# Performance work log

Hardware: AMD Instinct MI355X
Metric: run time of the kernel (lower is better)

## Reference

```python
import jax, jax.numpy as jnp
import numpy as np

C_NUM, D_NUM = 64, 128
N_NODES = C_NUM * D_NUM + C_NUM + D_NUM  # 8384
HEADS, OUT = 4, 256


def gat_conv(h, src, dst, W, al, ar, b):
    """DGL-style GATConv (eval mode, attn_drop off). h:[N,F], W:[F,H*O], al/ar:[H,O], b:[H*O]."""
    N = h.shape[0]
    H, O = al.shape
    feat = (h @ W).reshape(N, H, O)
    el = jnp.sum(feat * al, axis=-1)                      # [N,H]
    er = jnp.sum(feat * ar, axis=-1)
    e = jax.nn.leaky_relu(el[src] + er[dst], 0.2)         # [E,H]
    m = jax.ops.segment_max(e, dst, num_segments=N)
    m = jnp.where(jnp.isfinite(m), m, 0.0)
    p = jnp.exp(e - m[dst])
    s = jax.ops.segment_sum(p, dst, num_segments=N)
    a = p / jnp.maximum(s[dst], 1e-9)                     # edge softmax per dst, per head
    out = jax.ops.segment_sum(a[:, :, None] * feat[src], dst, num_segments=N)  # [N,H,O]
    return out + b.reshape(1, H, O)


def cagat_layer(edges, dfeat, cvec, gw, al, ar, gb,
                wq_w, wq_b, wk_w, wk_b, wv_w, wv_b, ip_w, ip_b, op_w, op_b):
    ch = cvec.shape[1]
    pad = jnp.repeat(cvec, D_NUM, axis=0)                       # [c*d, ch]
    pad3 = jnp.broadcast_to(cvec.mean(axis=0), (D_NUM, ch))      # [d, ch]
    cfin = jnp.concatenate([pad, cvec, pad3], axis=0)            # [N, ch]
    inf = jnp.concatenate([dfeat, cfin], axis=1)                 # [N, F+ch]
    # 4 relation-specific GATConvs, stacked (HeteroGraphConv aggregate='stack')
    rst = jnp.stack([gat_conv(inf, edges[t, 0], edges[t, 1], gw[t], al[t], ar[t], gb[t])
                     for t in range(4)], axis=1)                 # [N,4,H,O]
    N = inf.shape[0]
    rst = rst.reshape(N, 4 * HEADS, OUT)
    E = OUT
    Q = (cfin @ wq_w + wq_b)[:, None, :]                         # [N,1,E]
    K = rst @ wk_w + wk_b                                        # [N,16,E]
    V = rst @ wv_w + wv_b
    # nn.MultiheadAttention(E, 1): in-proj then single-head SDPA then out-proj
    q = Q @ ip_w[:E].T + ip_b[:E]
    k = K @ ip_w[E:2 * E].T + ip_b[E:2 * E]
    v = V @ ip_w[2 * E:].T + ip_b[2 * E:]
    att = jax.nn.softmax(jnp.einsum('nqe,nke->nqk', q, k) / jnp.sqrt(jnp.float32(E)), axis=-1)
    o = jnp.einsum('nqk,nke->nqe', att, v) @ op_w.T + op_b
    return o.reshape(N, E)


def setup_inputs() -> dict:
    key = jax.random.key(0)
    ks = iter(jax.random.split(key, 64))
    rn = lambda shape: jax.random.normal(next(ks), shape, jnp.float32) * 0.05
    inp = {}
    inp['x'] = rn((D_NUM, 256))
    inp['cf'] = rn((C_NUM, 512))
    inp['cf_net_w'] = rn((512, 128)); inp['cf_net_b'] = rn((128,))
    inp['ht_w'] = rn((512, 256)); inp['ht_b'] = rn((256,))
    for l in ('1', '2'):
        inp['gw' + l] = rn((4, 384, HEADS * OUT))
        inp['al' + l] = rn((4, HEADS, OUT))
        inp['ar' + l] = rn((4, HEADS, OUT))
        inp['gb' + l] = rn((4, HEADS * OUT))
        inp['wq' + l + '_w'] = rn((128, 256)); inp['wq' + l + '_b'] = rn((256,))
        inp['wk' + l + '_w'] = rn((256, 256)); inp['wk' + l + '_b'] = rn((256,))
        inp['wv' + l + '_w'] = rn((256, 256)); inp['wv' + l + '_b'] = rn((256,))
        inp['ip' + l + '_w'] = rn((768, 256)); inp['ip' + l + '_b'] = rn((768,))
        inp['op' + l + '_w'] = rn((256, 256)); inp['op' + l + '_b'] = rn((256,))
    inp['edges'] = jax.random.randint(next(ks), (4, 2, 50000), 0, N_NODES, dtype=jnp.int32)
    return inp


def reference(x, cf, cf_net_w, cf_net_b, ht_w, ht_b,
              gw1, al1, ar1, gb1, wq1_w, wq1_b, wk1_w, wk1_b, wv1_w, wv1_b, ip1_w, ip1_b, op1_w, op1_b,
              gw2, al2, ar2, gb2, wq2_w, wq2_b, wk2_w, wk2_b, wv2_w, wv2_b, ip2_w, ip2_b, op2_w, op2_b,
              edges):
    cf_vec = cf @ cf_net_w + cf_net_b                           # [c, cell_hidden]
    d_pad = jnp.tile(x, (C_NUM, 1))                             # [c*d, in]
    d_uc = cf @ ht_w + ht_b                                     # [c, in]
    d_feat = jnp.concatenate([d_pad, d_uc, x], axis=0)          # [N, in]
    h = cagat_layer(edges, d_feat, cf_vec, gw1, al1, ar1, gb1,
                    wq1_w, wq1_b, wk1_w, wk1_b, wv1_w, wv1_b, ip1_w, ip1_b, op1_w, op1_b)
    h = cagat_layer(edges, h, cf_vec, gw2, al2, ar2, gb2,
                    wq2_w, wq2_b, wk2_w, wk2_b, wv2_w, wv2_b, ip2_w, ip2_b, op2_w, op2_b)
    return h
```

## Files before the change

kernel.cpp:

```cpp
#include <hip/hip_runtime.h>
#include <hip/hip_bf16.h>

typedef __hip_bfloat16 bf16;
typedef __attribute__((ext_vector_type(8))) short short8;
typedef __attribute__((ext_vector_type(4))) short short4v;
typedef __attribute__((ext_vector_type(4))) float f32x4;

#define KN 8384
#define KNPAD 8448
#define KE 50000
#define NBIG 4480

__device__ __forceinline__ float toF(float v){ return v; }
__device__ __forceinline__ float toF(bf16 v){ return __bfloat162float(v); }
__device__ __forceinline__ float b2f(short u){ return __uint_as_float(((unsigned int)(unsigned short)u) << 16); }
__device__ __forceinline__ void stor(float* p, float v){ *p = v; }
__device__ __forceinline__ void stor(bf16* p, float v){ *p = __float2bfloat16(v); }

__device__ __forceinline__ void glds16(const bf16* g, bf16* l){
  __builtin_amdgcn_global_load_lds(
      (const __attribute__((address_space(1))) unsigned int*)(g),
      (__attribute__((address_space(3))) unsigned int*)(l), 16, 0, 0);
}

template<typename TC>
__global__ __launch_bounds__(256)
void gemm_mfma_bt(const bf16* __restrict__ A, const bf16* __restrict__ BT,
                  const float* __restrict__ bias, TC* __restrict__ C,
                  int M, int N, int K, int ldc)
{
  __shared__ bf16 As[128 * 32];
  __shared__ bf16 Bs[128 * 32];
  const int bm = blockIdx.y * 128, bn = blockIdx.x * 128;
  const int tid = threadIdx.x;
  const int w = tid >> 6, l = tid & 63;
  const int wr = (w >> 1) * 64, wc = (w & 1) * 64;
  const int lr = l & 15;
  int rS[2], lqS[2];
  #pragma unroll
  for (int i = 0; i < 2; i++){
    rS[i] = w * 32 + i * 16 + (l >> 2);
    lqS[i] = (l & 3) ^ ((rS[i] >> 1) & 3);
  }
  const bf16* gA0 = A  + (size_t)(bm + rS[0]) * K + lqS[0] * 8;
  const bf16* gA1 = A  + (size_t)(bm + rS[1]) * K + lqS[1] * 8;
  const bf16* gB0 = BT + (size_t)(bn + rS[0]) * K + lqS[0] * 8;
  const bf16* gB1 = BT + (size_t)(bn + rS[1]) * K + lqS[1] * 8;
  bf16* lA0 = &As[w * 1024];
  bf16* lA1 = &As[w * 1024 + 512];
  bf16* lB0 = &Bs[w * 1024];
  bf16* lB1 = &Bs[w * 1024 + 512];
  f32x4 acc[4][4] = {};
  for (int k0 = 0; k0 < K; k0 += 32) {
    glds16(gA0 + k0, lA0);
    glds16(gA1 + k0, lA1);
    glds16(gB0 + k0, lB0);
    glds16(gB1 + k0, lB1);
    __syncthreads();
    short8 a[4], b[4];
    #pragma unroll
    for (int i = 0; i < 4; i++){
      int R = wr + i * 16 + lr;
      int pq = (l >> 4) ^ ((R >> 1) & 3);
      a[i] = *(short8*)&As[R * 32 + pq * 8];
    }
    #pragma unroll
    for (int j = 0; j < 4; j++){
      int R = wc + j * 16 + lr;
      int pq = (l >> 4) ^ ((R >> 1) & 3);
      b[j] = *(short8*)&Bs[R * 32 + pq * 8];
    }
    #pragma unroll
    for (int i = 0; i < 4; i++)
      #pragma unroll
      for (int j = 0; j < 4; j++)
        acc[i][j] = __builtin_amdgcn_mfma_f32_16x16x32_bf16(a[i], b[j], acc[i][j], 0, 0, 0);
    __syncthreads();
  }
  const int orow = (l >> 4) * 4, ocol = l & 15;
  #pragma unroll
  for (int i = 0; i < 4; i++){
    #pragma unroll
    for (int j = 0; j < 4; j++){
      int gcol = bn + wc + j * 16 + ocol;
      float bv = bias ? bias[gcol] : 0.f;
      #pragma unroll
      for (int rg = 0; rg < 4; rg++){
        int grow = bm + wr + i * 16 + orow + rg;
        if (grow < M) stor(&C[(size_t)grow * ldc + gcol], acc[i][j][rg] + bv);
      }
    }
  }
}

__global__ void k_transGW(const float* __restrict__ gw, bf16* __restrict__ bigBT){
  __shared__ float t[32][33];
  int rel = blockIdx.z;
  const float* B = gw + (size_t)rel * 384 * 1024;
  bf16* BT = bigBT + (size_t)rel * 1024 * 384;
  int n0 = blockIdx.x * 32, k0 = blockIdx.y * 32;
  int tx = threadIdx.x, ty = threadIdx.y;
  for (int i = ty; i < 32; i += 8)
    t[i][tx] = B[(size_t)(k0 + i) * 1024 + n0 + tx];
  __syncthreads();
  for (int i = ty; i < 32; i += 8)
    BT[(size_t)(n0 + i) * 384 + k0 + tx] = __float2bfloat16(t[tx][i]);
}

__global__ __launch_bounds__(256)
void k_galr(const float* __restrict__ gw, const float* __restrict__ al,
            const float* __restrict__ ar, bf16* __restrict__ bigBT){
  int r = blockIdx.y;
  int k = blockIdx.x * 4 + (threadIdx.x >> 6);
  int lane = threadIdx.x & 63;
  int rr = r & 15, t = rr >> 2, h = rr & 3;
  const float* wsrc = ((r < 16) ? al : ar) + t * 1024 + h * 256;
  const float* gp = gw + (size_t)t * 384 * 1024 + (size_t)k * 1024 + h * 256;
  float v = 0.f;
  #pragma unroll
  for (int i = 0; i < 4; i++){
    int o = lane + i * 64;
    v += gp[o] * wsrc[o];
  }
  #pragma unroll
  for (int off = 32; off; off >>= 1) v += __shfl_down(v, off);
  if (lane == 0) bigBT[(size_t)(4352 + r) * 384 + k] = __float2bfloat16(v);
}

__global__ void k_zpad(bf16* bigBT){
  int i = blockIdx.x * blockDim.x + threadIdx.x;
  if (i < 96 * 384) bigBT[(size_t)4384 * 384 + i] = __float2bfloat16(0.f);
}

__global__ void k_wprep(const float* __restrict__ ipw, const float* __restrict__ wkw,
                        const float* __restrict__ opw, const float* __restrict__ wvw,
                        float* __restrict__ ipwQT, float* __restrict__ wkwT,
                        float* __restrict__ opwT, float* __restrict__ wvwT){
  __shared__ float t[32][33];
  const float* S; float* D;
  switch (blockIdx.z){
    case 0: S = ipw; D = ipwQT; break;
    case 1: S = wkw; D = wkwT; break;
    case 2: S = opw; D = opwT; break;
    default: S = wvw; D = wvwT; break;
  }
  int c0 = blockIdx.x * 32, r0 = blockIdx.y * 32;
  int tx = threadIdx.x, ty = threadIdx.y;
  for (int i = ty; i < 32; i += 8)
    t[i][tx] = S[(size_t)(r0 + i) * 256 + c0 + tx];
  __syncthreads();
  for (int i = ty; i < 32; i += 8)
    D[(size_t)(c0 + i) * 256 + r0 + tx] = t[tx][i];
}

__global__ __launch_bounds__(256)
void k_fold1(const float* __restrict__ wqw, const float* __restrict__ wqb,
             const float* __restrict__ ipw, const float* __restrict__ ipb,
             const float* __restrict__ ipwQT, const float* __restrict__ wkwT,
             const float* __restrict__ opwT,
             float* __restrict__ Wq, float* __restrict__ B2,
             float* __restrict__ M1, float* __restrict__ bq){
  int b = blockIdx.x, tid = threadIdx.x;
  if (b < 128){
    int c = b; float s = 0.f;
    for (int e = 0; e < 256; e++) s += wqw[c * 256 + e] * ipwQT[e * 256 + tid];
    Wq[c * 256 + tid] = s;
  } else if (b < 384){
    int j = b - 128; float s = 0.f;
    for (int e = 0; e < 256; e++) s += wkwT[e * 256 + tid] * ipw[(256 + j) * 256 + e];
    B2[j * 256 + tid] = s;
  } else if (b < 640){
    int e = b - 384; float s = 0.f;
    for (int f = 0; f < 256; f++) s += ipw[(512 + f) * 256 + e] * opwT[f * 256 + tid];
    M1[e * 256 + tid] = s;
  } else {
    float s = 0.f;
    for (int e = 0; e < 256; e++) s += wqb[e] * ipwQT[e * 256 + tid];
    bq[tid] = s + ipb[tid];
  }
}

__global__ __launch_bounds__(256)
void k_fold2(const float* __restrict__ Wq, const float* __restrict__ B2,
             const float* __restrict__ M1, const float* __restrict__ bq,
             const float* __restrict__ wvb, const float* __restrict__ ipb,
             const float* __restrict__ opb,
             const float* __restrict__ wvwT, const float* __restrict__ opwT,
             bf16* __restrict__ bigBT, bf16* __restrict__ WvT,
             float* __restrict__ bv, float* __restrict__ biasc){
  int b = blockIdx.x, tid = threadIdx.x;
  if (b < 256){
    int d = b; float s = 0.f;
    for (int j = 0; j < 256; j++) s += Wq[d * 256 + j] * B2[j * 256 + tid];
    bigBT[(size_t)(4096 + tid) * 384 + 256 + d] = __float2bfloat16(s);
  } else if (b < 512){
    int j = b - 256; float s = 0.f;
    for (int e = 0; e < 256; e++) s += wvwT[e * 256 + tid] * M1[e * 256 + j];
    WvT[j * 256 + tid] = __float2bfloat16(s);
  } else {
    float b2 = 0.f;
    for (int j = 0; j < 256; j++) b2 += bq[j] * B2[j * 256 + tid];
    float s = 0.f;
    for (int e = 0; e < 256; e++) s += wvb[e] * M1[e * 256 + tid];
    for (int f = 0; f < 256; f++) s += ipb[512 + f] * opwT[f * 256 + tid];
    bv[tid] = s + opb[tid];
    for (int i = tid; i < NBIG; i += 256)
      biasc[i] = (i - 4096 == tid) ? b2 : 0.f;
    for (int k = 0; k < 256; k++)
      bigBT[(size_t)(4096 + tid) * 384 + k] = __float2bfloat16(0.f);
  }
}

__global__ __launch_bounds__(384)
void k_pre(const float* __restrict__ cf, const float* __restrict__ cfw, const float* __restrict__ cfb,
           const float* __restrict__ htw, const float* __restrict__ htb,
           float* __restrict__ cfvec, float* __restrict__ duc)
{
  int c = blockIdx.x;
  int col = threadIdx.x;
  __shared__ float row[512];
  for (int i = col; i < 512; i += 384) row[i] = cf[c * 512 + i];
  __syncthreads();
  if (col < 128){
    float acc = cfb[col];
    for (int k = 0; k < 512; k++) acc += row[k] * cfw[k * 128 + col];
    cfvec[c * 128 + col] = acc;
  } else {
    int j = col - 128;
    float acc = htb[j];
    for (int k = 0; k < 512; k++) acc += row[k] * htw[k * 256 + j];
    duc[c * 256 + j] = acc;
  }
}
__global__ void k_mean(const float* cv, float* m){
  int o = threadIdx.x;
  float s = 0.f;
  for (int c = 0; c < 64; c++) s += cv[c * 128 + o];
  m[o] = s * (1.f / 64.f);
}
__global__ __launch_bounds__(384)
void k_infasm(const float* __restrict__ x, const float* __restrict__ duc,
              const float* __restrict__ cv, const float* __restrict__ cm,
              bf16* __restrict__ inf){
  int n = blockIdx.x, o = threadIdx.x;
  float v;
  if (o < 256){
    if (n < 8192)      v = x[(n & 127) * 256 + o];
    else if (n < 8256) v = duc[(n - 8192) * 256 + o];
    else               v = x[(n - 8256) * 256 + o];
  } else {
    int oo = o - 256;
    if (n < 8192)      v = cv[(n >> 7) * 128 + oo];
    else if (n < 8256) v = cv[(n - 8192) * 128 + oo];
    else               v = cm[oo];
  }
  inf[(size_t)n * 384 + o] = __float2bfloat16(v);
}
__global__ void k_zeroi(int* p, int n){
  int i = blockIdx.x * blockDim.x + threadIdx.x; if (i < n) p[i] = 0;
}
__global__ void k_copyi(const int* a, int* b, int n){
  int i = blockIdx.x * blockDim.x + threadIdx.x; if (i < n) b[i] = a[i];
}
__global__ void k_countB(const int* __restrict__ edges, int* __restrict__ cnt){
  int i = blockIdx.x * blockDim.x + threadIdx.x;
  if (i < 4 * KE){
    int t = i / KE, idx = i - t * KE;
    int d = edges[t * 2 * KE + KE + idx];
    atomicAdd(&cnt[t * KN + d], 1);
  }
}
__global__ void k_fillB(const int* __restrict__ edges, int* __restrict__ cur, int* __restrict__ csrc){
  int i = blockIdx.x * blockDim.x + threadIdx.x;
  if (i < 4 * KE){
    int t = i / KE, idx = i - t * KE;
    int s = edges[t * 2 * KE + idx];
    int d = edges[t * 2 * KE + KE + idx];
    int p = atomicAdd(&cur[t * KN + d], 1);
    csrc[p] = s;
  }
}
__global__ void k_scan(const int* __restrict__ cnt, int* __restrict__ ptr, int n){
  __shared__ int part[1024];
  int tid = threadIdx.x;
  const int CH = (n + 1023) >> 10;
  int base = tid * CH;
  int s = 0;
  for (int i = 0; i < CH; i++){ int idx = base + i; if (idx < n) s += cnt[idx]; }
  part[tid] = s; __syncthreads();
  for (int off = 1; off < 1024; off <<= 1){
    int v = (tid >= off) ? part[tid - off] : 0;
    __syncthreads();
    part[tid] += v;
    __syncthreads();
  }
  int run = part[tid] - s;
  for (int i = 0; i < CH; i++){
    int idx = base + i;
    if (idx < n){ ptr[idx] = run; run += cnt[idx]; }
  }
  if (tid == 1023) ptr[n] = part[1023];
}

__global__ __launch_bounds__(256)
void k_aggattn(const int* __restrict__ ptr, const int* __restrict__ csrc,
               const bf16* __restrict__ big, const float* __restrict__ gb,
               bf16* __restrict__ rbar)
{
  const int n = blockIdx.x, tid = threadIdx.x;
  const int w = tid >> 6, lane = tid & 63;
  const int t = w;
  const int head = lane >> 4;
  __shared__ float s_rst[16][260];
  __shared__ float s_sc[16];
  __shared__ float sa4[4][64][4];
  __shared__ int ssrcW[4][64];
  const int beg = ptr[t * KN + n], deg = ptr[t * KN + n + 1] - beg;
  short4v e4 = *(const short4v*)&big[(size_t)n * NBIG + 4368 + t * 4];
  float ern[4] = {b2f(e4[0]), b2f(e4[1]), b2f(e4[2]), b2f(e4[3])};
  float sums[4] = {0.f, 0.f, 0.f, 0.f};
  for (int j = lane; j < deg; j += 64){
    int s = csrc[beg + j];
    short4v l4 = *(const short4v*)&big[(size_t)s * NBIG + 4352 + t * 4];
    #pragma unroll
    for (int h = 0; h < 4; h++){
      float e = b2f(l4[h]) + ern[h];
      e = e > 0.f ? e : 0.2f * e;
      sums[h] += __expf(e);
    }
  }
  #pragma unroll
  for (int off = 32; off; off >>= 1){
    #pragma unroll
    for (int h = 0; h < 4; h++) sums[h] += __shfl_xor(sums[h], off);
  }
  float sinv[4];
  #pragma unroll
  for (int h = 0; h < 4; h++) sinv[h] = 1.f / fmaxf(sums[h], 1e-9f);
  float acc[16];
  #pragma unroll
  for (int i = 0; i < 16; i++) acc[i] = 0.f;
  const size_t cbase = (size_t)t * 1024 + lane * 16;
  for (int c0 = 0; c0 < deg; c0 += 64){
    int cn = min(64, deg - c0);
    if (lane < cn){
      int s = csrc[beg + c0 + lane];
      ssrcW[t][lane] = s;
      short4v l4 = *(const short4v*)&big[(size_t)s * NBIG + 4352 + t * 4];
      #pragma unroll
      for (int h = 0; h < 4; h++){
        float e = b2f(l4[h]) + ern[h];
        e = e > 0.f ? e : 0.2f * e;
        sa4[t][lane][h] = __expf(e) * sinv[h];
      }
    }
    for (int j = 0; j < cn; j++){
      int s = ssrcW[t][j];
      float wj = sa4[t][j][head];
      const bf16* fp = &big[(size_t)s * NBIG + cbase];
      short8 v0 = *(const short8*)fp;
      short8 v1 = *(const short8*)(fp + 8);
      #pragma unroll
      for (int i = 0; i < 8; i++) acc[i] += wj * b2f(v0[i]);
      #pragma unroll
      for (int i = 0; i < 8; i++) acc[8 + i] += wj * b2f(v1[i]);
    }
  }
  {
    const float* gbp = gb + t * 1024 + lane * 16;
    float* rp = &s_rst[t * 4 + head][(lane & 15) * 16];
    #pragma unroll
    for (int i = 0; i < 16; i++) rp[i] = acc[i] + gbp[i];
  }
  __syncthreads();
  const bf16* q = big + (size_t)n * NBIG + 4096;
  #pragma unroll
  for (int si = 0; si < 4; si++){
    int s = w * 4 + si;
    float v = 0.f;
    #pragma unroll
    for (int i = 0; i < 4; i++){
      int o = lane + i * 64;
      v += s_rst[s][o] * toF(q[o]);
    }
    #pragma unroll
    for (int off = 32; off; off >>= 1) v += __shfl_down(v, off);
    if (lane == 0) s_sc[s] = v * 0.0625f;
  }
  __syncthreads();
  float sc[16]; float m = -1e30f;
  #pragma unroll
  for (int s = 0; s < 16; s++){ sc[s] = s_sc[s]; m = fmaxf(m, sc[s]); }
  float sum = 0.f;
  #pragma unroll
  for (int s = 0; s < 16; s++){ sc[s] = __expf(sc[s] - m); sum += sc[s]; }
  float inv = 1.f / sum;
  float r = 0.f;
  #pragma unroll
  for (int s = 0; s < 16; s++) r += sc[s] * s_rst[s][tid];
  rbar[(size_t)n * 256 + tid] = __float2bfloat16(r * inv);
}

struct LWT {
  const float *gw, *al, *ar, *gb, *wqw, *wqb, *wkw, *wkb, *wvw, *wvb, *ipw, *ipb, *opw, *opb;
};

extern "C" void kernel_launch(void* const* d_in, const int* in_sizes, int n_in,
                              void* d_out, int out_size, void* d_ws, size_t ws_size,
                              hipStream_t stream)
{
  const float* x   = (const float*)d_in[0];
  const float* cf  = (const float*)d_in[1];
  const float* cfw = (const float*)d_in[2];
  const float* cfb = (const float*)d_in[3];
  const float* htw = (const float*)d_in[4];
  const float* htb = (const float*)d_in[5];
  LWT L[2];
  for (int l = 0; l < 2; l++){
    int b = 6 + l * 14;
    L[l].gw  = (const float*)d_in[b + 0];
    L[l].al  = (const float*)d_in[b + 1];
    L[l].ar  = (const float*)d_in[b + 2];
    L[l].gb  = (const float*)d_in[b + 3];
    L[l].wqw = (const float*)d_in[b + 4];
    L[l].wqb = (const float*)d_in[b + 5];
    L[l].wkw = (const float*)d_in[b + 6];
    L[l].wkb = (const float*)d_in[b + 7];
    L[l].wvw = (const float*)d_in[b + 8];
    L[l].wvb = (const float*)d_in[b + 9];
    L[l].ipw = (const float*)d_in[b + 10];
    L[l].ipb = (const float*)d_in[b + 11];
    L[l].opw = (const float*)d_in[b + 12];
    L[l].opb = (const float*)d_in[b + 13];
  }
  const int* edges = (const int*)d_in[34];

  char* w = (char*)d_ws;
  size_t off = 0;
  auto alc = [&](size_t bytes) -> void* {
    off = (off + 255) & ~(size_t)255;
    void* p = w + off; off += bytes; return p;
  };
  float* f_cfvec = (float*)alc(64 * 128 * 4);
  float* f_cfmean= (float*)alc(128 * 4);
  float* f_duc   = (float*)alc(64 * 256 * 4);
  bf16*  b_inf   = (bf16*) alc((size_t)KNPAD * 384 * 2);
  bf16*  b_big   = (bf16*) alc((size_t)KN * NBIG * 2);
  bf16*  b_bigBT = (bf16*) alc((size_t)NBIG * 384 * 2);
  float* f_biasc = (float*)alc((size_t)NBIG * 4);
  bf16*  b_rbar  = (bf16*) alc((size_t)KNPAD * 256 * 2);
  float* f_Wq    = (float*)alc(128 * 256 * 4);
  float* f_B2    = (float*)alc(256 * 256 * 4);
  float* f_M1    = (float*)alc(256 * 256 * 4);
  float* f_bq    = (float*)alc(256 * 4);
  float* f_bv    = (float*)alc(256 * 4);
  bf16*  b_WvT   = (bf16*) alc(256 * 256 * 2);
  float* f_ipwQT = (float*)alc(256 * 256 * 4);
  float* f_wkwT  = (float*)alc(256 * 256 * 4);
  float* f_opwT  = (float*)alc(256 * 256 * 4);
  float* f_wvwT  = (float*)alc(256 * 256 * 4);
  int*   i_ptr   = (int*)  alc((size_t)(4 * KN + 1) * 4);
  int*   i_src   = (int*)  alc((size_t)4 * KE * 4);
  int*   i_cnt   = (int*)  alc((size_t)4 * KN * 4);
  int*   i_cur   = (int*)  alc((size_t)4 * KN * 4);
  if (off > ws_size) return;

  k_pre<<<64, 384, 0, stream>>>(cf, cfw, cfb, htw, htb, f_cfvec, f_duc);
  k_mean<<<1, 128, 0, stream>>>(f_cfvec, f_cfmean);
  k_infasm<<<KN, 384, 0, stream>>>(x, f_duc, f_cfvec, f_cfmean, b_inf);
  k_zpad<<<(96 * 384 + 255) / 256, 256, 0, stream>>>(b_bigBT);

  k_zeroi<<<(4 * KN + 255) / 256, 256, 0, stream>>>(i_cnt, 4 * KN);
  k_countB<<<(4 * KE + 255) / 256, 256, 0, stream>>>(edges, i_cnt);
  k_scan<<<1, 1024, 0, stream>>>(i_cnt, i_ptr, 4 * KN);
  k_copyi<<<(4 * KN + 255) / 256, 256, 0, stream>>>(i_ptr, i_cur, 4 * KN);
  k_fillB<<<(4 * KE + 255) / 256, 256, 0, stream>>>(edges, i_cur, i_src);

  auto run_layer = [&](const LWT& Wt, bool last){
    k_transGW<<<dim3(32, 12, 4), dim3(32, 8), 0, stream>>>(Wt.gw, b_bigBT);
    k_galr<<<dim3(96, 32), 256, 0, stream>>>(Wt.gw, Wt.al, Wt.ar, b_bigBT);
    k_wprep<<<dim3(8, 8, 4), dim3(32, 8), 0, stream>>>(Wt.ipw, Wt.wkw, Wt.opw, Wt.wvw,
                                                       f_ipwQT, f_wkwT, f_opwT, f_wvwT);
    k_fold1<<<641, 256, 0, stream>>>(Wt.wqw, Wt.wqb, Wt.ipw, Wt.ipb,
                                     f_ipwQT, f_wkwT, f_opwT,
                                     f_Wq, f_B2, f_M1, f_bq);
    k_fold2<<<513, 256, 0, stream>>>(f_Wq, f_B2, f_M1, f_bq, Wt.wvb, Wt.ipb, Wt.opb,
                                     f_wvwT, f_opwT,
                                     b_bigBT, b_WvT, f_bv, f_biasc);
    gemm_mfma_bt<bf16><<<dim3(NBIG / 128, 66), 256, 0, stream>>>(
        b_inf, b_bigBT, f_biasc, b_big, KN, NBIG, 384, NBIG);
    k_aggattn<<<KN, 256, 0, stream>>>(i_ptr, i_src, b_big, Wt.gb, b_rbar);
    if (last)
      gemm_mfma_bt<float><<<dim3(2, 66), 256, 0, stream>>>(
          b_rbar, b_WvT, f_bv, (float*)d_out, KN, 256, 256, 256);
    else
      gemm_mfma_bt<bf16><<<dim3(2, 66), 256, 0, stream>>>(
          b_rbar, b_WvT, f_bv, b_inf, KN, 256, 256, 384);
  };

  run_layer(L[0], false);
  run_layer(L[1], true);
}
```

Before: 558.5 us.

## Triple-buffer GEMM LDS loads and remap workgroups across XCDs

```diff
diff --git a/kernel.cpp b/kernel.cpp
--- a/kernel.cpp
+++ b/kernel.cpp
@@ -27,11 +27,15 @@
 __global__ __launch_bounds__(256)
 void gemm_mfma_bt(const bf16* __restrict__ A, const bf16* __restrict__ BT,
                   const float* __restrict__ bias, TC* __restrict__ C,
-                  int M, int N, int K, int ldc)
+                  int M, int N, int K, int ldc, int nbx)
 {
-  __shared__ bf16 As[128 * 32];
-  __shared__ bf16 Bs[128 * 32];
-  const int bm = blockIdx.y * 128, bn = blockIdx.x * 128;
+  __shared__ bf16 As[3][128 * 32];
+  __shared__ bf16 Bs[3][128 * 32];
+  const int nwg = gridDim.x;
+  const int q = nwg >> 3, r = nwg & 7;
+  const int xcd = blockIdx.x & 7, idx = blockIdx.x >> 3;
+  const int sw = (xcd < r) ? xcd * (q + 1) + idx : r * (q + 1) + (xcd - r) * q + idx;
+  const int bn = (sw % nbx) * 128, bm = (sw / nbx) * 128;
   const int tid = threadIdx.x;
   const int w = tid >> 6, l = tid & 63;
   const int wr = (w >> 1) * 64, wc = (w & 1) * 64;
@@ -46,36 +50,41 @@
   const bf16* gA1 = A  + (size_t)(bm + rS[1]) * K + lqS[1] * 8;
   const bf16* gB0 = BT + (size_t)(bn + rS[0]) * K + lqS[0] * 8;
   const bf16* gB1 = BT + (size_t)(bn + rS[1]) * K + lqS[1] * 8;
-  bf16* lA0 = &As[w * 1024];
-  bf16* lA1 = &As[w * 1024 + 512];
-  bf16* lB0 = &Bs[w * 1024];
-  bf16* lB1 = &Bs[w * 1024 + 512];
+  const int nt = K >> 5;
+  auto issue = [&](int t){
+    int b = t - (t / 3) * 3;
+    int k0 = t << 5;
+    glds16(gA0 + k0, &As[b][w * 1024]);
+    glds16(gA1 + k0, &As[b][w * 1024 + 512]);
+    glds16(gB0 + k0, &Bs[b][w * 1024]);
+    glds16(gB1 + k0, &Bs[b][w * 1024 + 512]);
+  };
   f32x4 acc[4][4] = {};
-  for (int k0 = 0; k0 < K; k0 += 32) {
-    glds16(gA0 + k0, lA0);
-    glds16(gA1 + k0, lA1);
-    glds16(gB0 + k0, lB0);
-    glds16(gB1 + k0, lB1);
-    __syncthreads();
-    short8 a[4], b[4];
+  issue(0);
+  issue(1);
+  for (int t = 0; t < nt; t++){
+    if (t < nt - 1) asm volatile("s_waitcnt vmcnt(4)\ns_barrier" ::: "memory");
+    else            asm volatile("s_waitcnt vmcnt(0)\ns_barrier" ::: "memory");
+    int b = t - (t / 3) * 3;
+    short8 a[4], bb[4];
     #pragma unroll
     for (int i = 0; i < 4; i++){
       int R = wr + i * 16 + lr;
       int pq = (l >> 4) ^ ((R >> 1) & 3);
-      a[i] = *(short8*)&As[R * 32 + pq * 8];
+      a[i] = *(short8*)&As[b][R * 32 + pq * 8];
     }
     #pragma unroll
     for (int j = 0; j < 4; j++){
       int R = wc + j * 16 + lr;
       int pq = (l >> 4) ^ ((R >> 1) & 3);
-      b[j] = *(short8*)&Bs[R * 32 + pq * 8];
+      bb[j] = *(short8*)&Bs[b][R * 32 + pq * 8];
     }
     #pragma unroll
     for (int i = 0; i < 4; i++)
       #pragma unroll
       for (int j = 0; j < 4; j++)
-        acc[i][j] = __builtin_amdgcn_mfma_f32_16x16x32_bf16(a[i], b[j], acc[i][j], 0, 0, 0);
-    __syncthreads();
+        acc[i][j] = __builtin_amdgcn_mfma_f32_16x16x32_bf16(a[i], bb[j], acc[i][j], 0, 0, 0);
+    if (t + 2 < nt) issue(t + 2);
   }
   const int orow = (l >> 4) * 4, ocol = l & 15;
   #pragma unroll
@@ -487,15 +496,15 @@
     k_fold2<<<513, 256, 0, stream>>>(f_Wq, f_B2, f_M1, f_bq, Wt.wvb, Wt.ipb, Wt.opb,
                                      f_wvwT, f_opwT,
                                      b_bigBT, b_WvT, f_bv, f_biasc);
-    gemm_mfma_bt<bf16><<<dim3(NBIG / 128, 66), 256, 0, stream>>>(
-        b_inf, b_bigBT, f_biasc, b_big, KN, NBIG, 384, NBIG);
+    gemm_mfma_bt<bf16><<<(NBIG / 128) * 66, 256, 0, stream>>>(
+        b_inf, b_bigBT, f_biasc, b_big, KN, NBIG, 384, NBIG, NBIG / 128);
     k_aggattn<<<KN, 256, 0, stream>>>(i_ptr, i_src, b_big, Wt.gb, b_rbar);
     if (last)
-      gemm_mfma_bt<float><<<dim3(2, 66), 256, 0, stream>>>(
-          b_rbar, b_WvT, f_bv, (float*)d_out, KN, 256, 256, 256);
+      gemm_mfma_bt<float><<<2 * 66, 256, 0, stream>>>(
+          b_rbar, b_WvT, f_bv, (float*)d_out, KN, 256, 256, 256, 2);
     else
-      gemm_mfma_bt<bf16><<<dim3(2, 66), 256, 0, stream>>>(
-          b_rbar, b_WvT, f_bv, b_inf, KN, 256, 256, 384);
+      gemm_mfma_bt<bf16><<<2 * 66, 256, 0, stream>>>(
+          b_rbar, b_WvT, f_bv, b_inf, KN, 256, 256, 384, 2);
   };
 
   run_layer(L[0], false);
```

New measurement: 545.4 us. -2.3%, faster.
